# Optimization experiments

Measured on AMD Instinct MI355X. Metric: run time of the kernel, lower is better.

Reference implementation:

```python
import jax, jax.numpy as jnp
import numpy as np
import math

B, S, D, H = 2, 2048, 1024, 16
HD = D // H  # head_dim = 64

def setup_inputs() -> dict:
    key = jax.random.key(0)
    ks = jax.random.split(key, 11)
    def n(k, shape, scale=1.0):
        return jax.random.normal(k, shape, dtype=jnp.float32) * scale
    w_scale = 1.0 / math.sqrt(D)
    return {
        "q": n(ks[0], (B, S, D)),
        "k": n(ks[1], (B, S, D)),
        "v": n(ks[2], (B, S, D)),
        "WQ_w": n(ks[3], (D, D), w_scale),
        "WQ_b": n(ks[4], (D,), 0.01),
        "WK_w": n(ks[5], (D, D), w_scale),
        "WK_b": n(ks[6], (D,), 0.01),
        "WV_w": n(ks[7], (D, D), w_scale),
        "WV_b": n(ks[8], (D,), 0.01),
        "Wout_w": n(ks[9], (D, D), w_scale),
        "Wout_b": n(ks[10], (D,), 0.01),
    }

def reference(q, k, v, WQ_w, WQ_b, WK_w, WK_b, WV_w, WV_b, Wout_w, Wout_b):
    b, s, _ = k.shape
    # QKV projections (torch Linear: x @ W.T + b; here weights stored [in, out])
    qh = (q @ WQ_w + WQ_b).reshape(b, -1, H, HD).transpose(0, 2, 1, 3)  # [b,h,s,hd]
    kh = (k @ WK_w + WK_b).reshape(b, -1, H, HD).transpose(0, 2, 1, 3)
    vh = (v @ WV_w + WV_b).reshape(b, -1, H, HD).transpose(0, 2, 1, 3)
    # naive attention: full [b,h,s,s] score matrix
    scores = jnp.einsum("bhqd,bhkd->bhqk", qh, kh) / math.sqrt(HD)
    attn = jax.nn.softmax(scores, axis=-1)
    out = jnp.einsum("bhqk,bhkd->bhqd", attn, vh)
    concat = out.transpose(0, 2, 1, 3).reshape(b, -1, H * HD)  # [b,s,inner_dim]
    return concat @ Wout_w + Wout_b
```

## Files before the change

### kernel.cpp

```cpp
#include <hip/hip_runtime.h>
#include <hip/hip_bf16.h>
#include <stdint.h>

typedef __attribute__((ext_vector_type(8))) short bf16x8;
typedef __attribute__((ext_vector_type(4))) short short4v;
typedef __attribute__((ext_vector_type(4))) float f32x4;

#define MFMA16x16x32 __builtin_amdgcn_mfma_f32_16x16x32_bf16

__device__ __forceinline__ short f2b(float f) {
  union { float f; uint32_t u; } x;
  x.f = f;
  uint32_t u = x.u;
  uint32_t r = (u + 0x7FFFu + ((u >> 16) & 1u)) >> 16;
  return (short)(uint16_t)r;
}

__device__ __forceinline__ uint32_t cvt_pk_bf16(float lo, float hi) {
  uint32_t r;
  asm volatile("v_cvt_pk_bf16_f32 %0, %1, %2" : "=v"(r) : "v"(lo), "v"(hi));
  return r;
}
__device__ __forceinline__ float exp2_fast(float x) {
  float r;
  asm volatile("v_exp_f32 %0, %1" : "=v"(r) : "v"(x));
  return r;
}
__device__ __forceinline__ bf16x8 cvt8(const float4 a, const float4 b) {
  union { uint32_t u[4]; bf16x8 v; } o;
  o.u[0] = cvt_pk_bf16(a.x, a.y);
  o.u[1] = cvt_pk_bf16(a.z, a.w);
  o.u[2] = cvt_pk_bf16(b.x, b.y);
  o.u[3] = cvt_pk_bf16(b.z, b.w);
  return o.v;
}

__device__ __forceinline__ void async_copy16(const void* g, void* l) {
  __builtin_amdgcn_global_load_lds(
      (const __attribute__((address_space(1))) void*)g,
      (__attribute__((address_space(3))) void*)l, 16, 0, 0);
}

__global__ void prep_kernel(const float* __restrict__ W0,
                            const float* __restrict__ W1,
                            const float* __restrict__ W2,
                            const float* __restrict__ W3,
                            const float* __restrict__ q,
                            const float* __restrict__ k,
                            const float* __restrict__ v,
                            short* __restrict__ Wt,
                            short* __restrict__ xq,
                            short* __restrict__ xk,
                            short* __restrict__ xv) {
  __shared__ short tile[64][72];
  const int z = blockIdx.z;
  const int t = threadIdx.x;
  if (z < 4) {
    const float* W = (z == 0) ? W0 : (z == 1) ? W1 : (z == 2) ? W2 : W3;
    short* Wo = Wt + (size_t)z * 1024 * 1024;
    const int r0 = blockIdx.y * 64;
    const int c0 = blockIdx.x * 64;
#pragma unroll
    for (int i = 0; i < 4; ++i) {
      const int lin = i * 1024 + t * 4;
      const int r = lin >> 6, c = lin & 63;
      const float4 vv = *(const float4*)&W[(size_t)(r0 + r) * 1024 + c0 + c];
      tile[r][c + 0] = f2b(vv.x);
      tile[r][c + 1] = f2b(vv.y);
      tile[r][c + 2] = f2b(vv.z);
      tile[r][c + 3] = f2b(vv.w);
    }
    __syncthreads();
#pragma unroll
    for (int i = 0; i < 2; ++i) {
      const int lin = i * 2048 + t * 8;
      const int r = lin >> 6, c = lin & 63;
      bf16x8 ov;
#pragma unroll
      for (int jj = 0; jj < 8; ++jj) ov[jj] = tile[c + jj][r];
      *(bf16x8*)&Wo[(size_t)(c0 + r) * 1024 + r0 + c] = ov;
    }
  } else {
    const float* x = (z == 4) ? q : (z == 5) ? k : v;
    short* yp = (z == 4) ? xq : (z == 5) ? xk : xv;
    const int base = (blockIdx.y * 16 + blockIdx.x) * 256 + t;
#pragma unroll
    for (int j = 0; j < 8; ++j) {
      const int i = base + j * 65536;
      const float4 a = ((const float4*)x)[2 * i];
      const float4 b = ((const float4*)x)[2 * i + 1];
      ((bf16x8*)yp)[i] = cvt8(a, b);
    }
  }
}

__launch_bounds__(256, 2)
__global__ void gemm_qkv_kernel(const short* __restrict__ A0,
                                const short* __restrict__ A1,
                                const short* __restrict__ A2,
                                const short* __restrict__ WtBase,
                                const float* __restrict__ b0,
                                const float* __restrict__ b1,
                                const float* __restrict__ b2,
                                short* __restrict__ C0,
                                short* __restrict__ C1,
                                short* __restrict__ Vt,
                                int ybase) {
  const int K = 1024;
  __shared__ short As[128 * 64];
  __shared__ short Bs[128 * 64];

  const int y = blockIdx.y + ybase;
  const short* A = (y == 0) ? A0 : (y == 1) ? A1 : A2;
  const short* Wt = WtBase + (size_t)y * 1024 * 1024;
  const float* bias = (y == 0) ? b0 : (y == 1) ? b1 : b2;

  const int tm = blockIdx.x & 31;
  const int tn = blockIdx.x >> 5;
  const int m0 = tm * 128, n0 = tn * 128;

  const int tid = threadIdx.x;
  const int lane = tid & 63;
  const int w = tid >> 6;
  const int wr = w >> 1, wc = w & 1;
  const int hi = lane >> 4, cc = lane & 15;
  const int srow = lane >> 3, schunk = lane & 7;

  f32x4 acc[4][4] = {};

  for (int kt = 0; kt < 16; ++kt) {
    const int k0 = kt * 64;
#pragma unroll
    for (int i = 0; i < 4; ++i) {
      const int ri = w * 4 + i;
      const int row = ri * 8 + srow;
      const int gch = schunk ^ (row & 7);
      async_copy16(A + (size_t)(m0 + row) * K + (k0 + gch * 8), &As[ri * 512]);
      async_copy16(Wt + (size_t)(n0 + row) * K + (k0 + gch * 8), &Bs[ri * 512]);
    }
    __syncthreads();
#pragma unroll
    for (int kk = 0; kk < 2; ++kk) {
      bf16x8 af[4], bfr[4];
#pragma unroll
      for (int x = 0; x < 4; ++x) {
        const int gch = kk * 4 + hi;
        const int rowA = wr * 64 + x * 16 + cc;
        af[x] = *(const bf16x8*)&As[rowA * 64 + ((gch ^ (rowA & 7)) << 3)];
        const int rowB = wc * 64 + x * 16 + cc;
        bfr[x] = *(const bf16x8*)&Bs[rowB * 64 + ((gch ^ (rowB & 7)) << 3)];
      }
#pragma unroll
      for (int x = 0; x < 4; ++x)
#pragma unroll
        for (int yy = 0; yy < 4; ++yy)
          acc[x][yy] = MFMA16x16x32(af[x], bfr[yy], acc[x][yy], 0, 0, 0);
    }
    __syncthreads();
  }

  short* Cout = (y == 0) ? C0 : C1;
#pragma unroll
  for (int x = 0; x < 4; ++x) {
    const int rbase = m0 + wr * 64 + x * 16 + (hi << 2);
#pragma unroll
    for (int yy = 0; yy < 4; ++yy) {
      const int col = n0 + wc * 64 + yy * 16 + cc;
      const float bv = bias[col];
      if (y == 2) {
        const int b = rbase >> 11, s = rbase & 2047;
        const int hh = col >> 6, d = col & 63;
        short4v pack;
#pragma unroll
        for (int r = 0; r < 4; ++r) pack[r] = f2b(acc[x][yy][r] + bv);
        *(short4v*)&Vt[((size_t)(b * 16 + hh) * 64 + d) * 2048 + s] = pack;
      } else {
#pragma unroll
        for (int r = 0; r < 4; ++r)
          Cout[(size_t)(rbase + r) * 1024 + col] = f2b(acc[x][yy][r] + bv);
      }
    }
  }
}

__launch_bounds__(256, 2)
__global__ void gemm_out_kernel(const short* __restrict__ A,
                                const short* __restrict__ Wt,
                                const float* __restrict__ bias,
                                float* __restrict__ C) {
  const int N = 1024, K = 1024;
  __shared__ short As[128 * 64];
  __shared__ short Bs[128 * 64];

  const int tm = blockIdx.x & 31;
  const int tn = blockIdx.x >> 5;
  const int m0 = tm * 128, n0 = tn * 128;

  const int tid = threadIdx.x;
  const int lane = tid & 63;
  const int w = tid >> 6;
  const int wr = w >> 1, wc = w & 1;
  const int hi = lane >> 4, cc = lane & 15;
  const int srow = lane >> 3, schunk = lane & 7;

  f32x4 acc[4][4] = {};

  for (int kt = 0; kt < 16; ++kt) {
    const int k0 = kt * 64;
#pragma unroll
    for (int i = 0; i < 4; ++i) {
      const int ri = w * 4 + i;
      const int row = ri * 8 + srow;
      const int gch = schunk ^ (row & 7);
      async_copy16(A + (size_t)(m0 + row) * K + (k0 + gch * 8), &As[ri * 512]);
      async_copy16(Wt + (size_t)(n0 + row) * K + (k0 + gch * 8), &Bs[ri * 512]);
    }
    __syncthreads();
#pragma unroll
    for (int kk = 0; kk < 2; ++kk) {
      bf16x8 af[4], bfr[4];
#pragma unroll
      for (int x = 0; x < 4; ++x) {
        const int gch = kk * 4 + hi;
        const int rowA = wr * 64 + x * 16 + cc;
        af[x] = *(const bf16x8*)&As[rowA * 64 + ((gch ^ (rowA & 7)) << 3)];
        const int rowB = wc * 64 + x * 16 + cc;
        bfr[x] = *(const bf16x8*)&Bs[rowB * 64 + ((gch ^ (rowB & 7)) << 3)];
      }
#pragma unroll
      for (int x = 0; x < 4; ++x)
#pragma unroll
        for (int yy = 0; yy < 4; ++yy)
          acc[x][yy] = MFMA16x16x32(af[x], bfr[yy], acc[x][yy], 0, 0, 0);
    }
    __syncthreads();
  }

#pragma unroll
  for (int x = 0; x < 4; ++x) {
    const int rbase = m0 + wr * 64 + x * 16 + (hi << 2);
#pragma unroll
    for (int yy = 0; yy < 4; ++yy) {
      const int col = n0 + wc * 64 + yy * 16 + cc;
      const float bv = bias[col];
#pragma unroll
      for (int r = 0; r < 4; ++r)
        C[(size_t)(rbase + r) * N + col] = acc[x][yy][r] + bv;
    }
  }
}

__launch_bounds__(256, 2)
__global__ void attn_kernel(const short* __restrict__ qh,
                            const short* __restrict__ kh,
                            const short* __restrict__ Vt,
                            short* __restrict__ concat) {
  const int S = 2048;
  const float CL2 = 0.18033688011112042f;
  __shared__ short Ks[2][64 * 64];
  __shared__ short Vs[2][64 * 64];
  __shared__ short Ps[4 * 32 * 64];

  const int qb = blockIdx.x;
  const int h = blockIdx.y;
  const int b = blockIdx.z;
  const int tid = threadIdx.x, lane = tid & 63, w = tid >> 6;
  const int hi = lane >> 4, cc = lane & 15;

  const size_t rowbase = (size_t)b * S;
  const int q0 = qb * 128 + w * 32;

  bf16x8 qf[2][2];
#pragma unroll
  for (int aq = 0; aq < 2; ++aq)
#pragma unroll
    for (int kk = 0; kk < 2; ++kk) {
      const int col = h * 64 + kk * 32 + hi * 8;
      qf[aq][kk] =
          *(const bf16x8*)&qh[(rowbase + q0 + aq * 16 + cc) * 1024 + col];
    }

  f32x4 oacc[2][4] = {};
  float l[2] = {0.f, 0.f};

  const short* Vth = Vt + (size_t)(b * 16 + h) * 64 * 2048;
  short* Pw = &Ps[w * 2048];
  const int srow = lane >> 3, schunk = lane & 7;
  const int e0 = (cc >> 3) & 1;

#pragma unroll
  for (int i = 0; i < 2; ++i) {
    const int ri = w * 2 + i;
    const int row = ri * 8 + srow;
    const int gch = schunk ^ (row & 7);
    async_copy16(&kh[(rowbase + row) * 1024 + h * 64 + gch * 8], &Ks[0][ri * 512]);
    async_copy16(&Vth[(size_t)row * 2048 + gch * 8], &Vs[0][ri * 512]);
  }
  __syncthreads();

  for (int t = 0; t < S / 64; ++t) {
    const int cur = t & 1;
    if (t + 1 < S / 64) {
      const int kv0 = (t + 1) * 64;
#pragma unroll
      for (int i = 0; i < 2; ++i) {
        const int ri = w * 2 + i;
        const int row = ri * 8 + srow;
        const int gch = schunk ^ (row & 7);
        async_copy16(&kh[(rowbase + kv0 + row) * 1024 + h * 64 + gch * 8],
                     &Ks[cur ^ 1][ri * 512]);
        async_copy16(&Vth[(size_t)row * 2048 + kv0 + gch * 8],
                     &Vs[cur ^ 1][ri * 512]);
      }
    }

    f32x4 sacc[2][4] = {};
#pragma unroll
    for (int kk = 0; kk < 2; ++kk) {
      bf16x8 kf[4];
#pragma unroll
      for (int n = 0; n < 4; ++n) {
        const int row = n * 16 + cc;
        const int ch = (kk * 4 + hi) ^ (cc & 7);
        kf[n] = *(const bf16x8*)&Ks[cur][row * 64 + (ch << 3)];
      }
#pragma unroll
      for (int aq = 0; aq < 2; ++aq)
#pragma unroll
        for (int n = 0; n < 4; ++n)
          sacc[aq][n] = MFMA16x16x32(kf[n], qf[aq][kk], sacc[aq][n], 0, 0, 0);
    }

#pragma unroll
    for (int aq = 0; aq < 2; ++aq) {
      const int qrow = aq * 16 + cc;
#pragma unroll
      for (int n = 0; n < 4; ++n) {
        const float p0 = exp2_fast(sacc[aq][n][0] * CL2);
        const float p1 = exp2_fast(sacc[aq][n][1] * CL2);
        const float p2 = exp2_fast(sacc[aq][n][2] * CL2);
        const float p3 = exp2_fast(sacc[aq][n][3] * CL2);
        l[aq] += (p0 + p1) + (p2 + p3);
        const uint32_t u0 = cvt_pk_bf16(p0, p1);
        const uint32_t u1 = cvt_pk_bf16(p2, p3);
        const int chunk = (2 * n + (hi >> 1)) ^ (cc & 7);
        const int base = qrow * 64 + (chunk << 3) + ((hi & 1) << 2);
        *(uint32_t*)&Pw[base + (e0 << 1)] = e0 ? u1 : u0;
        *(uint32_t*)&Pw[base + ((e0 ^ 1) << 1)] = e0 ? u0 : u1;
      }
    }

#pragma unroll
    for (int kvh = 0; kvh < 2; ++kvh) {
      const int ch = (kvh * 4 + hi) ^ (cc & 7);
      bf16x8 pf[2], vf[4];
#pragma unroll
      for (int aq = 0; aq < 2; ++aq)
        pf[aq] = *(const bf16x8*)&Pw[(aq * 16 + cc) * 64 + (ch << 3)];
#pragma unroll
      for (int n = 0; n < 4; ++n) {
        const int row = n * 16 + cc;
        vf[n] = *(const bf16x8*)&Vs[cur][row * 64 + (ch << 3)];
      }
#pragma unroll
      for (int aq = 0; aq < 2; ++aq)
#pragma unroll
        for (int n = 0; n < 4; ++n)
          oacc[aq][n] = MFMA16x16x32(vf[n], pf[aq], oacc[aq][n], 0, 0, 0);
    }
    __syncthreads();
  }

#pragma unroll
  for (int aq = 0; aq < 2; ++aq) {
    float lv = l[aq];
    lv += __shfl_xor(lv, 16);
    lv += __shfl_xor(lv, 32);
    const float inv = 1.0f / lv;
    const size_t grow = rowbase + q0 + aq * 16 + cc;
#pragma unroll
    for (int n = 0; n < 4; ++n)
#pragma unroll
      for (int r = 0; r < 4; ++r) {
        const int d = n * 16 + hi * 4 + r;
        concat[grow * 1024 + h * 64 + d] = f2b(oacc[aq][n][r] * inv);
      }
  }
}

extern "C" void kernel_launch(void* const* d_in, const int* in_sizes, int n_in,
                              void* d_out, int out_size, void* d_ws, size_t ws_size,
                              hipStream_t stream) {
  const float* q = (const float*)d_in[0];
  const float* k = (const float*)d_in[1];
  const float* v = (const float*)d_in[2];
  const float* WQ = (const float*)d_in[3];
  const float* bQ = (const float*)d_in[4];
  const float* WK = (const float*)d_in[5];
  const float* bK = (const float*)d_in[6];
  const float* WV = (const float*)d_in[7];
  const float* bV = (const float*)d_in[8];
  const float* WO = (const float*)d_in[9];
  const float* bO = (const float*)d_in[10];

  char* ws = (char*)d_ws;
  const size_t MB = 1024 * 1024;
  short* Wt = (short*)ws;
  short* xq = (short*)(ws + 8 * MB);
  short* xk = (short*)(ws + 16 * MB);
  short* xv = (short*)(ws + 24 * MB);
  short* qh = (short*)(ws + 32 * MB);
  short* kh = (short*)(ws + 40 * MB);
  short* concat = xk;

  prep_kernel<<<dim3(16, 16, 7), 256, 0, stream>>>(WQ, WK, WV, WO, q, k, v,
                                                   Wt, xq, xk, xv);

  if (ws_size >= 56 * MB) {
    short* Vt = (short*)(ws + 48 * MB);
    gemm_qkv_kernel<<<dim3(256, 3), 256, 0, stream>>>(
        xq, xk, xv, Wt, bQ, bK, bV, qh, kh, Vt, 0);
    attn_kernel<<<dim3(16, 16, 2), 256, 0, stream>>>(qh, kh, Vt, concat);
  } else {
    short* Vt = xq;
    gemm_qkv_kernel<<<dim3(256, 2), 256, 0, stream>>>(
        xq, xk, xv, Wt, bQ, bK, bV, qh, kh, Vt, 0);
    gemm_qkv_kernel<<<dim3(256, 1), 256, 0, stream>>>(
        xq, xk, xv, Wt, bQ, bK, bV, qh, kh, Vt, 2);
    attn_kernel<<<dim3(16, 16, 2), 256, 0, stream>>>(qh, kh, Vt, concat);
  }

  gemm_out_kernel<<<256, 256, 0, stream>>>(concat, Wt + 3 * MB, bO,
                                           (float*)d_out);
}
```

Before: 126.3 us.

## Software-pipeline attention loop to overlap QK of tile t with PV of t-1

Restructures the attention KV loop into a skewed software pipeline. Each iteration computes QK scores for the current tile while doing the P·V matmul for the previous tile. V fragments are held in registers across the iteration boundary, and the P scratch buffer in shared memory is double-buffered so the two stages do not conflict. The goal is to break the serial QK→softmax→PV dependency chain inside each iteration and give the scheduler independent MFMA work to interleave with the exp and convert instructions. The cost is higher register pressure and twice the LDS for P, which could reduce occupancy.

```diff
diff --git a/kernel.cpp b/kernel.cpp
--- a/kernel.cpp
+++ b/kernel.cpp
@@ -255,11 +255,10 @@
                             const short* __restrict__ kh,
                             const short* __restrict__ Vt,
                             short* __restrict__ concat) {
-  const int S = 2048;
   const float CL2 = 0.18033688011112042f;
   __shared__ short Ks[2][64 * 64];
   __shared__ short Vs[2][64 * 64];
-  __shared__ short Ps[4 * 32 * 64];
+  __shared__ short Ps[2][4 * 32 * 64];
 
   const int qb = blockIdx.x;
   const int h = blockIdx.y;
@@ -267,7 +266,7 @@
   const int tid = threadIdx.x, lane = tid & 63, w = tid >> 6;
   const int hi = lane >> 4, cc = lane & 15;
 
-  const size_t rowbase = (size_t)b * S;
+  const size_t rowbase = (size_t)b * 2048;
   const int q0 = qb * 128 + w * 32;
 
   bf16x8 qf[2][2];
@@ -282,39 +281,25 @@
 
   f32x4 oacc[2][4] = {};
   float l[2] = {0.f, 0.f};
+  bf16x8 vf[2][4];
 
   const short* Vth = Vt + (size_t)(b * 16 + h) * 64 * 2048;
-  short* Pw = &Ps[w * 2048];
   const int srow = lane >> 3, schunk = lane & 7;
   const int e0 = (cc >> 3) & 1;
 
-#pragma unroll
-  for (int i = 0; i < 2; ++i) {
-    const int ri = w * 2 + i;
-    const int row = ri * 8 + srow;
-    const int gch = schunk ^ (row & 7);
-    async_copy16(&kh[(rowbase + row) * 1024 + h * 64 + gch * 8], &Ks[0][ri * 512]);
-    async_copy16(&Vth[(size_t)row * 2048 + gch * 8], &Vs[0][ri * 512]);
-  }
-  __syncthreads();
-
-  for (int t = 0; t < S / 64; ++t) {
-    const int cur = t & 1;
-    if (t + 1 < S / 64) {
-      const int kv0 = (t + 1) * 64;
-#pragma unroll
-      for (int i = 0; i < 2; ++i) {
-        const int ri = w * 2 + i;
-        const int row = ri * 8 + srow;
-        const int gch = schunk ^ (row & 7);
-        async_copy16(&kh[(rowbase + kv0 + row) * 1024 + h * 64 + gch * 8],
-                     &Ks[cur ^ 1][ri * 512]);
-        async_copy16(&Vth[(size_t)row * 2048 + kv0 + gch * 8],
-                     &Vs[cur ^ 1][ri * 512]);
-      }
-    }
-
-    f32x4 sacc[2][4] = {};
+  auto STAGE = [&](int tile, int buf) {
+#pragma unroll
+    for (int i = 0; i < 2; ++i) {
+      const int ri = w * 2 + i;
+      const int row = ri * 8 + srow;
+      const int gch = schunk ^ (row & 7);
+      async_copy16(&kh[(rowbase + tile * 64 + row) * 1024 + h * 64 + gch * 8],
+                   &Ks[buf][ri * 512]);
+      async_copy16(&Vth[(size_t)row * 2048 + tile * 64 + gch * 8],
+                   &Vs[buf][ri * 512]);
+    }
+  };
+  auto QK = [&](int buf, f32x4 (&sacc)[2][4]) {
 #pragma unroll
     for (int kk = 0; kk < 2; ++kk) {
       bf16x8 kf[4];
@@ -322,7 +307,7 @@
       for (int n = 0; n < 4; ++n) {
         const int row = n * 16 + cc;
         const int ch = (kk * 4 + hi) ^ (cc & 7);
-        kf[n] = *(const bf16x8*)&Ks[cur][row * 64 + (ch << 3)];
+        kf[n] = *(const bf16x8*)&Ks[buf][row * 64 + (ch << 3)];
       }
 #pragma unroll
       for (int aq = 0; aq < 2; ++aq)
@@ -330,7 +315,19 @@
         for (int n = 0; n < 4; ++n)
           sacc[aq][n] = MFMA16x16x32(kf[n], qf[aq][kk], sacc[aq][n], 0, 0, 0);
     }
-
+  };
+  auto LOADV = [&](int buf) {
+#pragma unroll
+    for (int kvh = 0; kvh < 2; ++kvh) {
+      const int ch = (kvh * 4 + hi) ^ (cc & 7);
+#pragma unroll
+      for (int n = 0; n < 4; ++n)
+        vf[kvh][n] =
+            *(const bf16x8*)&Vs[buf][(n * 16 + cc) * 64 + (ch << 3)];
+    }
+  };
+  auto SOFTMAX = [&](f32x4 (&sacc)[2][4], int slot) {
+    short* Pp = &Ps[slot][w * 2048];
 #pragma unroll
     for (int aq = 0; aq < 2; ++aq) {
       const int qrow = aq * 16 + cc;
@@ -345,31 +342,50 @@
         const uint32_t u1 = cvt_pk_bf16(p2, p3);
         const int chunk = (2 * n + (hi >> 1)) ^ (cc & 7);
         const int base = qrow * 64 + (chunk << 3) + ((hi & 1) << 2);
-        *(uint32_t*)&Pw[base + (e0 << 1)] = e0 ? u1 : u0;
-        *(uint32_t*)&Pw[base + ((e0 ^ 1) << 1)] = e0 ? u0 : u1;
-      }
-    }
-
+        *(uint32_t*)&Pp[base + (e0 << 1)] = e0 ? u1 : u0;
+        *(uint32_t*)&Pp[base + ((e0 ^ 1) << 1)] = e0 ? u0 : u1;
+      }
+    }
+  };
+  auto PV = [&](int slot) {
+    const short* Pp = &Ps[slot][w * 2048];
 #pragma unroll
     for (int kvh = 0; kvh < 2; ++kvh) {
       const int ch = (kvh * 4 + hi) ^ (cc & 7);
-      bf16x8 pf[2], vf[4];
+      bf16x8 pf[2];
 #pragma unroll
       for (int aq = 0; aq < 2; ++aq)
-        pf[aq] = *(const bf16x8*)&Pw[(aq * 16 + cc) * 64 + (ch << 3)];
-#pragma unroll
-      for (int n = 0; n < 4; ++n) {
-        const int row = n * 16 + cc;
-        vf[n] = *(const bf16x8*)&Vs[cur][row * 64 + (ch << 3)];
-      }
+        pf[aq] = *(const bf16x8*)&Pp[(aq * 16 + cc) * 64 + (ch << 3)];
 #pragma unroll
       for (int aq = 0; aq < 2; ++aq)
 #pragma unroll
         for (int n = 0; n < 4; ++n)
-          oacc[aq][n] = MFMA16x16x32(vf[n], pf[aq], oacc[aq][n], 0, 0, 0);
-    }
-    __syncthreads();
-  }
+          oacc[aq][n] = MFMA16x16x32(vf[kvh][n], pf[aq], oacc[aq][n], 0, 0, 0);
+    }
+  };
+
+  STAGE(0, 0);
+  __syncthreads();
+  {
+    STAGE(1, 1);
+    f32x4 sacc[2][4] = {};
+    QK(0, sacc);
+    LOADV(0);
+    SOFTMAX(sacc, 0);
+    __syncthreads();
+  }
+
+  for (int t = 1; t < 32; ++t) {
+    const int cur = t & 1;
+    if (t + 1 < 32) STAGE(t + 1, cur ^ 1);
+    f32x4 sacc[2][4] = {};
+    QK(cur, sacc);
+    PV(cur ^ 1);
+    LOADV(cur);
+    SOFTMAX(sacc, cur);
+    __syncthreads();
+  }
+  PV(1);
 
 #pragma unroll
   for (int aq = 0; aq < 2; ++aq) {
```

Result: faster. 123.3 us (-2.4%).
